# Performance work log

Hardware: AMD Instinct MI355X
Metric: run time of the kernel (lower is better)

Reference implementation:

```python
import jax, jax.numpy as jnp
import numpy as np

N_QUBITS = 8
N_LAYERS = 3
N_CLASSES = 3
BATCH = 16384


def setup_inputs() -> dict:
    key = jax.random.key(0)
    k1, k2, k3, k4 = jax.random.split(key, 4)
    x = jax.random.uniform(k1, (BATCH, N_QUBITS), dtype=jnp.float32)  # PCA feats in [0,1]
    q_weights = jax.random.normal(k2, (N_LAYERS * 2 * N_QUBITS,), dtype=jnp.float32) * 0.1
    W = jax.random.normal(k3, (N_CLASSES, N_CLASSES), dtype=jnp.float32) / np.sqrt(N_CLASSES)
    b = jax.random.normal(k4, (N_CLASSES,), dtype=jnp.float32) * 0.1
    return {"x": x, "q_weights": q_weights, "W": W, "b": b}


def _ry(state, wire, theta):
    """Batched RY(theta) on `wire`. state: (B,)+(2,)*n, theta: (B,)."""
    ax = 1 + wire
    s0 = jnp.take(state, 0, axis=ax)
    s1 = jnp.take(state, 1, axis=ax)
    bshape = (theta.shape[0],) + (1,) * (s0.ndim - 1)
    c = jnp.cos(0.5 * theta).reshape(bshape)
    s = jnp.sin(0.5 * theta).reshape(bshape)
    return jnp.stack([c * s0 - s * s1, s * s0 + c * s1], axis=ax)


def _rz(state, wire, theta):
    """RZ(theta) on `wire`, theta scalar: diag(e^{-i t/2}, e^{i t/2})."""
    ax = 1 + wire
    phases = jnp.stack([jnp.exp(-0.5j * theta), jnp.exp(0.5j * theta)])
    shape = (1,) * ax + (2,) + (1,) * (state.ndim - ax - 1)
    return state * phases.reshape(shape)


def _cnot(state, ctrl, tgt):
    """CNOT: flip target bit on the control=1 slice."""
    cax = 1 + ctrl
    a0 = jnp.take(state, 0, axis=cax)
    a1 = jnp.take(state, 1, axis=cax)
    # control axis was removed; target axis shifts down by one if tgt > ctrl
    tax = 1 + tgt if tgt < ctrl else tgt
    a1 = jnp.flip(a1, axis=tax)
    return jnp.stack([a0, a1], axis=cax)


def _circuit(x, q_weights):
    B = x.shape[0]
    state = jnp.zeros((B, 2 ** N_QUBITS), dtype=jnp.complex64).at[:, 0].set(1.0)
    state = state.reshape((B,) + (2,) * N_QUBITS)
    for layer in range(N_LAYERS):
        base = layer * 2 * N_QUBITS
        for i in range(N_QUBITS):
            state = _ry(state, i, x[:, i] * np.pi + q_weights[base + i])
        for i in range(N_QUBITS - 1):
            state = _cnot(state, i, i + 1)
        state = _cnot(state, N_QUBITS - 1, 0)
        for i in range(N_QUBITS):
            state = _rz(state, i, q_weights[base + N_QUBITS + i])
    probs = state.real ** 2 + state.imag ** 2  # (B,)+(2,)*n
    zs = []
    for i in range(N_CLASSES):
        ax = 1 + i
        p = probs.sum(axis=tuple(a for a in range(1, N_QUBITS + 1) if a != ax))  # (B,2)
        zs.append(p[:, 0] - p[:, 1])  # <Z_i>
    return jnp.stack(zs, axis=1).astype(jnp.float32)  # (B, n_classes)


def reference(x, q_weights, W, b):
    q_out = _circuit(x, q_weights)
    return q_out @ W.T + b
```

## Files before the change

### kernel.cpp

```cpp
#include <hip/hip_runtime.h>
#include <math.h>

#define NQ 8
#define NL 3
#define NC 3
#define BATCH 16384


__device__ __forceinline__ int par(int x) { return __popc(x) & 1; }

template<int CTRL>
__device__ __forceinline__ float dppmov(float v) {
  return __builtin_bit_cast(float,
    __builtin_amdgcn_update_dpp(0, __builtin_bit_cast(int, v), CTRL, 0xF, 0xF, true));
}

template<int M>
__device__ __forceinline__ float xl(float v) {
  if constexpr (M >= 16) {
    return __builtin_bit_cast(float,
      __builtin_amdgcn_ds_swizzle(__builtin_bit_cast(int, v), (M << 10) | 0x1F));
  } else {
    constexpr int hi = M & 12;
    constexpr int first = (hi == 0) ? 0 : (hi == 4) ? 0x141
                          : (hi == 8) ? 0x128
                          : 0x140;
    constexpr int qx = (hi == 4 || hi == 12) ? ((M & 3) ^ 3) : (M & 3);
    constexpr int qc = (qx == 1) ? 0xB1 : (qx == 2) ? 0x4E : 0x1B;
    float t = v;
    if constexpr (first != 0) t = dppmov<first>(t);
    if constexpr (qx != 0)    t = dppmov<qc>(t);
    return t;
  }
}

template<int UREG, int GREG, int GLANE>
__device__ __forceinline__ void ry_rr(float (&sr)[8], float (&si)[8],
                                      float c, float s, int q) {
  const float sl = par(q & GLANE) ? s : -s;
  #pragma unroll
  for (int rA = 0; rA < 8; ++rA) {
    if (rA < (rA ^ UREG)) {
      const int rB = rA ^ UREG;
      const float FA = par(rA & GREG) ? -sl : sl;
      const float ar = sr[rA], ai = si[rA];
      sr[rA] = c * ar + FA * sr[rB];
      si[rA] = c * ai + FA * si[rB];
      sr[rB] = c * sr[rB] - FA * ar;
      si[rB] = c * si[rB] - FA * ai;
    }
  }
}

template<int ULANE, int GREG, int GLANE>
__device__ __forceinline__ void ry_ll(float (&sr)[8], float (&si)[8],
                                      float c, float s, int q) {
  const float sl = par(q & GLANE) ? s : -s;
  #pragma unroll
  for (int r = 0; r < 8; ++r) {
    const float xr = xl<ULANE>(sr[r]);
    const float xi = xl<ULANE>(si[r]);
    const float F  = par(r & GREG) ? -sl : sl;
    sr[r] = c * sr[r] + F * xr;
    si[r] = c * si[r] + F * xi;
  }
}

template<int UREG, int ULANE, int GREG, int GLANE>
__device__ __forceinline__ void ry_mix(float (&sr)[8], float (&si)[8],
                                       float c, float s, int q) {
  constexpr int RFLIP = __builtin_popcount(GREG & UREG) & 1;
  const float sl = par(q & GLANE) ? s : -s;
  #pragma unroll
  for (int rA = 0; rA < 8; ++rA) {
    if (rA < (rA ^ UREG)) {
      const int rB = rA ^ UREG;
      const float pBr = xl<ULANE>(sr[rB]);
      const float pBi = xl<ULANE>(si[rB]);
      const float pAr = xl<ULANE>(sr[rA]);
      const float pAi = xl<ULANE>(si[rA]);
      const float FA = par(rA & GREG) ? -sl : sl;
      const float FB = RFLIP ? -FA : FA;
      sr[rA] = c * sr[rA] + FA * pBr;
      si[rA] = c * si[rA] + FA * pBi;
      sr[rB] = c * sr[rB] + FB * pAr;
      si[rB] = c * si[rB] + FB * pAi;
    }
  }
}

__global__ __launch_bounds__(256, 8) void vqc_kernel(
    const float* __restrict__ x, const float* __restrict__ qw,
    const float* __restrict__ W, const float* __restrict__ b,
    float* __restrict__ out)
{
  const int tid  = threadIdx.x;
  const int q    = tid & 31;
  const int elem = blockIdx.x * 8 + (tid >> 5);

  const float PI = 3.14159265358979323846f;

  float xs[8];
  {
    const float4 x0 = *(const float4*)(x + elem * 8);
    const float4 x1 = *(const float4*)(x + elem * 8 + 4);
    xs[0] = x0.x; xs[1] = x0.y; xs[2] = x0.z; xs[3] = x0.w;
    xs[4] = x1.x; xs[5] = x1.y; xs[6] = x1.z; xs[7] = x1.w;
  }

  float sr[8], si[8];

  {
    float cw[8], sv[8];
    #pragma unroll
    for (int w = 0; w < 8; ++w)
      __sincosf(0.5f * (PI * xs[w] + qw[w]), &sv[w], &cw[w]);

    float P = ((q & 1)  ? sv[3] : cw[3]);
    P      *= ((q & 2)  ? sv[4] : cw[4]);
    P      *= ((q & 4)  ? sv[5] : cw[5]);
    P      *= ((q & 8)  ? sv[6] : cw[6]);
    P      *= ((q & 16) ? sv[7] : cw[7]);
    sr[0] = P * cw[0];
    sr[1] = P * sv[0];
    #pragma unroll
    for (int r = 0; r < 2; ++r) { sr[r + 2] = sr[r] * sv[1]; sr[r] *= cw[1]; }
    #pragma unroll
    for (int r = 0; r < 4; ++r) { sr[r + 4] = sr[r] * sv[2]; sr[r] *= cw[2]; }
  }

  {
    const float h0 = 0.5f * qw[8],  h1 = 0.5f * qw[9];
    const float h2 = 0.5f * qw[10], h3 = 0.5f * qw[11];
    const float h4 = 0.5f * qw[12], h5 = 0.5f * qw[13];
    const float h6 = 0.5f * qw[14], h7 = 0.5f * qw[15];
    const float a0 = par(q & 31) ? h0 : -h0;
    const float a1 = -h1;
    const float A7 = -h2 + (par(q & 1)  ? h3 : -h3) + (par(q & 3)  ? h4 : -h4)
                         + (par(q & 7)  ? h5 : -h5) + (par(q & 15) ? h6 : -h6)
                         + (par(q & 31) ? h7 : -h7);
    float cp[8], sp[8];
    #pragma unroll
    for (int r = 0; r < 8; ++r) {
      if (!(r & 2)) {
        const float phi = (par(r & 6) ? -a0 : a0) + (par(r & 3) ? -a1 : a1)
                        + (par(r & 7) ? -A7 : A7);
        float s_, c_;
        __sincosf(phi, &s_, &c_);
        cp[r] = c_;     sp[r] = s_;
        cp[r ^ 2] = c_; sp[r ^ 2] = -s_;
      }
    }
    #pragma unroll
    for (int r = 0; r < 8; ++r) { si[r] = sp[r] * sr[r]; sr[r] = cp[r] * sr[r]; }
  }

  {
    float cw[8], sv[8];
    #pragma unroll
    for (int w = 0; w < 8; ++w)
      __sincosf(0.5f * (PI * xs[w] + qw[16 + w]), &sv[w], &cw[w]);

    ry_rr <3,     6, 31>(sr, si, cw[0], sv[0], q);
    ry_rr <6,     3,  0>(sr, si, cw[1], sv[1], q);
    ry_mix<4, 1,  7,  0>(sr, si, cw[2], sv[2], q);
    ry_ll <3,     7,  1>(sr, si, cw[3], sv[3], q);
    ry_ll <6,     7,  3>(sr, si, cw[4], sv[4], q);
    ry_ll <12,    7,  7>(sr, si, cw[5], sv[5], q);
    ry_ll <24,    7, 15>(sr, si, cw[6], sv[6], q);
    ry_mix<3, 16, 7, 31>(sr, si, cw[7], sv[7], q);
  }

  {
    const float h0 = 0.5f * qw[24], h1 = 0.5f * qw[25];
    const float h2 = 0.5f * qw[26], h3 = 0.5f * qw[27];
    const float h4 = 0.5f * qw[28], h5 = 0.5f * qw[29];
    const float h6 = 0.5f * qw[30], h7 = 0.5f * qw[31];
    const float a0 = par(q & 21) ? h0 : -h0;
    const float A5 = (par(q & 31) ? h1 : -h1) + (par(q & 30) ? h3 : -h3)
                   + (par(q & 26) ? h5 : -h5) + (par(q & 10) ? h7 : -h7);
    const float A2 = (par(q & 31) ? h2 : -h2) + (par(q & 29) ? h4 : -h4)
                   + (par(q & 21) ? h6 : -h6);
    float cp[8], sp[8];
    #pragma unroll
    for (int r = 0; r < 4; ++r) {
      const float phi = (par(r & 3) ? -a0 : a0) + (par(r & 5) ? -A5 : A5)
                      + (par(r & 2) ? -A2 : A2);
      float s_, c_;
      __sincosf(phi, &s_, &c_);
      cp[r] = c_;     sp[r] = s_;
      cp[r ^ 6] = c_; sp[r ^ 6] = -s_;
    }
    #pragma unroll
    for (int r = 0; r < 8; ++r) {
      const float re = sr[r], im = si[r];
      sr[r] = cp[r] * re - sp[r] * im;
      si[r] = cp[r] * im + sp[r] * re;
    }
  }

  {
    float cw[8], sv[8];
    #pragma unroll
    for (int w = 0; w < 8; ++w)
      __sincosf(0.5f * (PI * xs[w] + qw[32 + w]), &sv[w], &cw[w]);

    ry_rr <5,     3, 21>(sr, si, cw[0], sv[0], q);
    ry_mix<2, 1,  5, 31>(sr, si, cw[1], sv[1], q);
    ry_mix<4, 2,  2, 31>(sr, si, cw[2], sv[2], q);
    ry_ll <5,     5, 30>(sr, si, cw[3], sv[3], q);
    ry_ll <10,    2, 29>(sr, si, cw[4], sv[4], q);
    ry_ll <20,    5, 26>(sr, si, cw[5], sv[5], q);
    ry_mix<3, 8,  2, 21>(sr, si, cw[6], sv[6], q);
    ry_mix<6, 16, 5, 10>(sr, si, cw[7], sv[7], q);
  }

  float z0 = 0.f, z1 = 0.f, z2 = 0.f;
  #pragma unroll
  for (int r = 0; r < 8; ++r) {
    const float p = sr[r] * sr[r] + si[r] * si[r];
    z0 += par(r & 2) ? -p : p;
    z1 += par(r & 6) ? -p : p;
    z2 += par(r & 4) ? -p : p;
  }
  if (par(q & 6))  z0 = -z0;
  if (par(q & 10)) z1 = -z1;
  if (par(q & 21)) z2 = -z2;

  z0 += xl<1>(z0);  z1 += xl<1>(z1);  z2 += xl<1>(z2);
  z0 += xl<2>(z0);  z1 += xl<2>(z1);  z2 += xl<2>(z2);
  z0 += xl<4>(z0);  z1 += xl<4>(z1);  z2 += xl<4>(z2);
  z0 += xl<8>(z0);  z1 += xl<8>(z1);  z2 += xl<8>(z2);
  z0 += xl<16>(z0); z1 += xl<16>(z1); z2 += xl<16>(z2);

  if (q < NC) {
    out[elem * NC + q] = b[q] + W[q * 3 + 0] * z0 + W[q * 3 + 1] * z1
                              + W[q * 3 + 2] * z2;
  }
}

extern "C" void kernel_launch(void* const* d_in, const int* in_sizes, int n_in,
                              void* d_out, int out_size, void* d_ws, size_t ws_size,
                              hipStream_t stream) {
  const float* x  = (const float*)d_in[0];
  const float* qw = (const float*)d_in[1];
  const float* W  = (const float*)d_in[2];
  const float* b  = (const float*)d_in[3];
  float* out = (float*)d_out;

  dim3 grid(BATCH / 8);
  vqc_kernel<<<grid, 256, 0, stream>>>(x, qw, W, b, out);
}
```

Baseline: 22.94 us.

## Split state 16 registers x 16 lanes per batch element, drop ds_swizzle

Changes the per-element statevector layout from 8 registers across 32 lanes to 16 registers across 16 lanes, so every cross-lane exchange is done with DPP alone and the ds_swizzle path goes away. The gate wire mappings and phase and sign bookkeeping are redone for the new split, and each block now handles 16 batch elements. Launch bounds drop to 4 waves per SIMD to allow the larger register footprint. This trades fewer lane exchanges and more per-thread ILP for higher register pressure and lower occupancy.

```diff
diff --git a/kernel.cpp b/kernel.cpp
--- a/kernel.cpp
+++ b/kernel.cpp
@@ -17,32 +17,30 @@
 
 template<int M>
 __device__ __forceinline__ float xl(float v) {
-  if constexpr (M >= 16) {
-    return __builtin_bit_cast(float,
-      __builtin_amdgcn_ds_swizzle(__builtin_bit_cast(int, v), (M << 10) | 0x1F));
-  } else {
-    constexpr int hi = M & 12;
-    constexpr int first = (hi == 0) ? 0 : (hi == 4) ? 0x141
-                          : (hi == 8) ? 0x128
-                          : 0x140;
-    constexpr int qx = (hi == 4 || hi == 12) ? ((M & 3) ^ 3) : (M & 3);
-    constexpr int qc = (qx == 1) ? 0xB1 : (qx == 2) ? 0x4E : 0x1B;
-    float t = v;
-    if constexpr (first != 0) t = dppmov<first>(t);
-    if constexpr (qx != 0)    t = dppmov<qc>(t);
-    return t;
-  }
-}
+  static_assert(M > 0 && M < 16, "DPP-only exchange");
+  constexpr int hi = M & 12;
+  constexpr int first = (hi == 0) ? 0 : (hi == 4) ? 0x141
+                        : (hi == 8) ? 0x128
+                        : 0x140;
+  constexpr int qx = (hi == 4 || hi == 12) ? ((M & 3) ^ 3) : (M & 3);
+  constexpr int qc = (qx == 1) ? 0xB1 : (qx == 2) ? 0x4E : 0x1B;
+  float t = v;
+  if constexpr (first != 0) t = dppmov<first>(t);
+  if constexpr (qx != 0)    t = dppmov<qc>(t);
+  return t;
+}
+
 
 template<int UREG, int GREG, int GLANE>
-__device__ __forceinline__ void ry_rr(float (&sr)[8], float (&si)[8],
+__device__ __forceinline__ void ry_rr(float (&sr)[16], float (&si)[16],
                                       float c, float s, int q) {
+  static_assert((__builtin_popcount(UREG & GREG) & 1) == 1, "<g,u>!=1");
   const float sl = par(q & GLANE) ? s : -s;
   #pragma unroll
-  for (int rA = 0; rA < 8; ++rA) {
+  for (int rA = 0; rA < 16; ++rA) {
     if (rA < (rA ^ UREG)) {
       const int rB = rA ^ UREG;
-      const float FA = par(rA & GREG) ? -sl : sl;
+      const float FA = (__builtin_popcount(rA & GREG) & 1) ? -sl : sl;
       const float ar = sr[rA], ai = si[rA];
       sr[rA] = c * ar + FA * sr[rB];
       si[rA] = c * ai + FA * si[rB];
@@ -53,33 +51,36 @@
 }
 
 template<int ULANE, int GREG, int GLANE>
-__device__ __forceinline__ void ry_ll(float (&sr)[8], float (&si)[8],
+__device__ __forceinline__ void ry_ll(float (&sr)[16], float (&si)[16],
                                       float c, float s, int q) {
+  static_assert((__builtin_popcount(ULANE & GLANE) & 1) == 1, "<g,u>!=1");
   const float sl = par(q & GLANE) ? s : -s;
   #pragma unroll
-  for (int r = 0; r < 8; ++r) {
+  for (int r = 0; r < 16; ++r) {
     const float xr = xl<ULANE>(sr[r]);
     const float xi = xl<ULANE>(si[r]);
-    const float F  = par(r & GREG) ? -sl : sl;
+    const float F  = (__builtin_popcount(r & GREG) & 1) ? -sl : sl;
     sr[r] = c * sr[r] + F * xr;
     si[r] = c * si[r] + F * xi;
   }
 }
 
 template<int UREG, int ULANE, int GREG, int GLANE>
-__device__ __forceinline__ void ry_mix(float (&sr)[8], float (&si)[8],
+__device__ __forceinline__ void ry_mix(float (&sr)[16], float (&si)[16],
                                        float c, float s, int q) {
+  static_assert(((__builtin_popcount(UREG & GREG) + __builtin_popcount(ULANE & GLANE)) & 1) == 1,
+                "<g,u>!=1");
   constexpr int RFLIP = __builtin_popcount(GREG & UREG) & 1;
   const float sl = par(q & GLANE) ? s : -s;
   #pragma unroll
-  for (int rA = 0; rA < 8; ++rA) {
+  for (int rA = 0; rA < 16; ++rA) {
     if (rA < (rA ^ UREG)) {
       const int rB = rA ^ UREG;
       const float pBr = xl<ULANE>(sr[rB]);
       const float pBi = xl<ULANE>(si[rB]);
       const float pAr = xl<ULANE>(sr[rA]);
       const float pAi = xl<ULANE>(si[rA]);
-      const float FA = par(rA & GREG) ? -sl : sl;
+      const float FA = (__builtin_popcount(rA & GREG) & 1) ? -sl : sl;
       const float FB = RFLIP ? -FA : FA;
       sr[rA] = c * sr[rA] + FA * pBr;
       si[rA] = c * si[rA] + FA * pBi;
@@ -89,14 +90,14 @@
   }
 }
 
-__global__ __launch_bounds__(256, 8) void vqc_kernel(
+__global__ __launch_bounds__(256, 4) void vqc_kernel(
     const float* __restrict__ x, const float* __restrict__ qw,
     const float* __restrict__ W, const float* __restrict__ b,
     float* __restrict__ out)
 {
   const int tid  = threadIdx.x;
-  const int q    = tid & 31;
-  const int elem = blockIdx.x * 8 + (tid >> 5);
+  const int q    = tid & 15;
+  const int elem = blockIdx.x * 16 + (tid >> 4);
 
   const float PI = 3.14159265358979323846f;
 
@@ -108,25 +109,26 @@
     xs[4] = x1.x; xs[5] = x1.y; xs[6] = x1.z; xs[7] = x1.w;
   }
 
-  float sr[8], si[8];
-
-  {
-    float cw[8], sv[8];
+  float sr[16], si[16];
+
+  {
+    float cw[8], sw[8];
     #pragma unroll
     for (int w = 0; w < 8; ++w)
-      __sincosf(0.5f * (PI * xs[w] + qw[w]), &sv[w], &cw[w]);
-
-    float P = ((q & 1)  ? sv[3] : cw[3]);
-    P      *= ((q & 2)  ? sv[4] : cw[4]);
-    P      *= ((q & 4)  ? sv[5] : cw[5]);
-    P      *= ((q & 8)  ? sv[6] : cw[6]);
-    P      *= ((q & 16) ? sv[7] : cw[7]);
+      __sincosf(0.5f * (PI * xs[w] + qw[w]), &sw[w], &cw[w]);
+
+    float P = ((q & 1) ? sw[4] : cw[4]);
+    P      *= ((q & 2) ? sw[5] : cw[5]);
+    P      *= ((q & 4) ? sw[6] : cw[6]);
+    P      *= ((q & 8) ? sw[7] : cw[7]);
     sr[0] = P * cw[0];
-    sr[1] = P * sv[0];
-    #pragma unroll
-    for (int r = 0; r < 2; ++r) { sr[r + 2] = sr[r] * sv[1]; sr[r] *= cw[1]; }
-    #pragma unroll
-    for (int r = 0; r < 4; ++r) { sr[r + 4] = sr[r] * sv[2]; sr[r] *= cw[2]; }
+    sr[1] = P * sw[0];
+    #pragma unroll
+    for (int r = 0; r < 2; ++r) { sr[r + 2] = sr[r] * sw[1]; sr[r] *= cw[1]; }
+    #pragma unroll
+    for (int r = 0; r < 4; ++r) { sr[r + 4] = sr[r] * sw[2]; sr[r] *= cw[2]; }
+    #pragma unroll
+    for (int r = 0; r < 8; ++r) { sr[r + 8] = sr[r] * sw[3]; sr[r] *= cw[3]; }
   }
 
   {
@@ -134,17 +136,19 @@
     const float h2 = 0.5f * qw[10], h3 = 0.5f * qw[11];
     const float h4 = 0.5f * qw[12], h5 = 0.5f * qw[13];
     const float h6 = 0.5f * qw[14], h7 = 0.5f * qw[15];
-    const float a0 = par(q & 31) ? h0 : -h0;
-    const float a1 = -h1;
-    const float A7 = -h2 + (par(q & 1)  ? h3 : -h3) + (par(q & 3)  ? h4 : -h4)
-                         + (par(q & 7)  ? h5 : -h5) + (par(q & 15) ? h6 : -h6)
-                         + (par(q & 31) ? h7 : -h7);
-    float cp[8], sp[8];
-    #pragma unroll
-    for (int r = 0; r < 8; ++r) {
+    const float c0 = par(q & 15) ? h0 : -h0;
+    const float c1 = -h1;
+    const float c2 = -h2;
+    const float A  = -h3 + (par(q & 1) ? h4 : -h4) + (par(q & 3)  ? h5 : -h5)
+                         + (par(q & 7) ? h6 : -h6) + (par(q & 15) ? h7 : -h7);
+    float cp[16], sp[16];
+    #pragma unroll
+    for (int r = 0; r < 16; ++r) {
       if (!(r & 2)) {
-        const float phi = (par(r & 6) ? -a0 : a0) + (par(r & 3) ? -a1 : a1)
-                        + (par(r & 7) ? -A7 : A7);
+        const float phi = ((__builtin_popcount(r & 14) & 1) ? -c0 : c0)
+                        + ((__builtin_popcount(r & 3)  & 1) ? -c1 : c1)
+                        + ((__builtin_popcount(r & 7)  & 1) ? -c2 : c2)
+                        + ((__builtin_popcount(r & 15) & 1) ? -A  : A);
         float s_, c_;
         __sincosf(phi, &s_, &c_);
         cp[r] = c_;     sp[r] = s_;
@@ -152,23 +156,23 @@
       }
     }
     #pragma unroll
-    for (int r = 0; r < 8; ++r) { si[r] = sp[r] * sr[r]; sr[r] = cp[r] * sr[r]; }
-  }
-
-  {
-    float cw[8], sv[8];
+    for (int r = 0; r < 16; ++r) { si[r] = sp[r] * sr[r]; sr[r] = cp[r] * sr[r]; }
+  }
+
+  {
+    float cw[8], sw[8];
     #pragma unroll
     for (int w = 0; w < 8; ++w)
-      __sincosf(0.5f * (PI * xs[w] + qw[16 + w]), &sv[w], &cw[w]);
-
-    ry_rr <3,     6, 31>(sr, si, cw[0], sv[0], q);
-    ry_rr <6,     3,  0>(sr, si, cw[1], sv[1], q);
-    ry_mix<4, 1,  7,  0>(sr, si, cw[2], sv[2], q);
-    ry_ll <3,     7,  1>(sr, si, cw[3], sv[3], q);
-    ry_ll <6,     7,  3>(sr, si, cw[4], sv[4], q);
-    ry_ll <12,    7,  7>(sr, si, cw[5], sv[5], q);
-    ry_ll <24,    7, 15>(sr, si, cw[6], sv[6], q);
-    ry_mix<3, 16, 7, 31>(sr, si, cw[7], sv[7], q);
+      __sincosf(0.5f * (PI * xs[w] + qw[16 + w]), &sw[w], &cw[w]);
+
+    ry_rr <3,    14, 15>(sr, si, cw[0], sw[0], q);
+    ry_rr <6,     3,  0>(sr, si, cw[1], sw[1], q);
+    ry_rr <12,    7,  0>(sr, si, cw[2], sw[2], q);
+    ry_mix<8, 1, 15,  0>(sr, si, cw[3], sw[3], q);
+    ry_ll <3,    15,  1>(sr, si, cw[4], sw[4], q);
+    ry_ll <6,    15,  3>(sr, si, cw[5], sw[5], q);
+    ry_ll <12,   15,  7>(sr, si, cw[6], sw[6], q);
+    ry_mix<3, 8, 15, 15>(sr, si, cw[7], sw[7], q);
   }
 
   {
@@ -176,23 +180,28 @@
     const float h2 = 0.5f * qw[26], h3 = 0.5f * qw[27];
     const float h4 = 0.5f * qw[28], h5 = 0.5f * qw[29];
     const float h6 = 0.5f * qw[30], h7 = 0.5f * qw[31];
-    const float a0 = par(q & 21) ? h0 : -h0;
-    const float A5 = (par(q & 31) ? h1 : -h1) + (par(q & 30) ? h3 : -h3)
-                   + (par(q & 26) ? h5 : -h5) + (par(q & 10) ? h7 : -h7);
-    const float A2 = (par(q & 31) ? h2 : -h2) + (par(q & 29) ? h4 : -h4)
-                   + (par(q & 21) ? h6 : -h6);
-    float cp[8], sp[8];
-    #pragma unroll
-    for (int r = 0; r < 4; ++r) {
-      const float phi = (par(r & 3) ? -a0 : a0) + (par(r & 5) ? -A5 : A5)
-                      + (par(r & 2) ? -A2 : A2);
-      float s_, c_;
-      __sincosf(phi, &s_, &c_);
-      cp[r] = c_;     sp[r] = s_;
-      cp[r ^ 6] = c_; sp[r ^ 6] = -s_;
-    }
-    #pragma unroll
-    for (int r = 0; r < 8; ++r) {
+    const float d0 = par(q & 10) ? h0 : -h0;
+    const float d1 = par(q & 15) ? h1 : -h1;
+    const float d2 = (par(q & 15) ? h2 : -h2) + (par(q & 14) ? h4 : -h4)
+                   + (par(q & 10) ? h6 : -h6);
+    const float d3 = (par(q & 15) ? h3 : -h3) + (par(q & 13) ? h5 : -h5)
+                   + (par(q & 5)  ? h7 : -h7);
+    float cp[16], sp[16];
+    #pragma unroll
+    for (int r = 0; r < 16; ++r) {
+      if (!(r & 2)) {
+        const float phi = ((__builtin_popcount(r & 11) & 1) ? -d0 : d0)
+                        + ((__builtin_popcount(r & 13) & 1) ? -d1 : d1)
+                        + ((__builtin_popcount(r & 10) & 1) ? -d2 : d2)
+                        + ((__builtin_popcount(r & 5)  & 1) ? -d3 : d3);
+        float s_, c_;
+        __sincosf(phi, &s_, &c_);
+        cp[r] = c_;     sp[r] = s_;
+        cp[r ^ 6] = c_; sp[r ^ 6] = -s_;
+      }
+    }
+    #pragma unroll
+    for (int r = 0; r < 16; ++r) {
       const float re = sr[r], im = si[r];
       sr[r] = cp[r] * re - sp[r] * im;
       si[r] = cp[r] * im + sp[r] * re;
@@ -200,38 +209,37 @@
   }
 
   {
-    float cw[8], sv[8];
+    float cw[8], sw[8];
     #pragma unroll
     for (int w = 0; w < 8; ++w)
-      __sincosf(0.5f * (PI * xs[w] + qw[32 + w]), &sv[w], &cw[w]);
-
-    ry_rr <5,     3, 21>(sr, si, cw[0], sv[0], q);
-    ry_mix<2, 1,  5, 31>(sr, si, cw[1], sv[1], q);
-    ry_mix<4, 2,  2, 31>(sr, si, cw[2], sv[2], q);
-    ry_ll <5,     5, 30>(sr, si, cw[3], sv[3], q);
-    ry_ll <10,    2, 29>(sr, si, cw[4], sv[4], q);
-    ry_ll <20,    5, 26>(sr, si, cw[5], sv[5], q);
-    ry_mix<3, 8,  2, 21>(sr, si, cw[6], sv[6], q);
-    ry_mix<6, 16, 5, 10>(sr, si, cw[7], sv[7], q);
+      __sincosf(0.5f * (PI * xs[w] + qw[32 + w]), &sw[w], &cw[w]);
+
+    ry_rr <5,    11, 10>(sr, si, cw[0], sw[0], q);
+    ry_rr <10,   13, 15>(sr, si, cw[1], sw[1], q);
+    ry_mix<4, 1, 10, 15>(sr, si, cw[2], sw[2], q);
+    ry_mix<8, 2,  5, 15>(sr, si, cw[3], sw[3], q);
+    ry_ll <5,    10, 14>(sr, si, cw[4], sw[4], q);
+    ry_ll <10,    5, 13>(sr, si, cw[5], sw[5], q);
+    ry_mix<3, 4, 10, 10>(sr, si, cw[6], sw[6], q);
+    ry_mix<6, 8,  5,  5>(sr, si, cw[7], sw[7], q);
   }
 
   float z0 = 0.f, z1 = 0.f, z2 = 0.f;
   #pragma unroll
-  for (int r = 0; r < 8; ++r) {
+  for (int r = 0; r < 16; ++r) {
     const float p = sr[r] * sr[r] + si[r] * si[r];
-    z0 += par(r & 2) ? -p : p;
-    z1 += par(r & 6) ? -p : p;
-    z2 += par(r & 4) ? -p : p;
-  }
-  if (par(q & 6))  z0 = -z0;
-  if (par(q & 10)) z1 = -z1;
-  if (par(q & 21)) z2 = -z2;
-
-  z0 += xl<1>(z0);  z1 += xl<1>(z1);  z2 += xl<1>(z2);
-  z0 += xl<2>(z0);  z1 += xl<2>(z1);  z2 += xl<2>(z2);
-  z0 += xl<4>(z0);  z1 += xl<4>(z1);  z2 += xl<4>(z2);
-  z0 += xl<8>(z0);  z1 += xl<8>(z1);  z2 += xl<8>(z2);
-  z0 += xl<16>(z0); z1 += xl<16>(z1); z2 += xl<16>(z2);
+    z0 += (__popc(r & 2)  & 1) ? -p : p;
+    z1 += (__popc(r & 6)  & 1) ? -p : p;
+    z2 += (__popc(r & 12) & 1) ? -p : p;
+  }
+  if (par(q & 3))  z0 = -z0;
+  if (par(q & 5))  z1 = -z1;
+  if (par(q & 10)) z2 = -z2;
+
+  z0 += xl<1>(z0); z1 += xl<1>(z1); z2 += xl<1>(z2);
+  z0 += xl<2>(z0); z1 += xl<2>(z1); z2 += xl<2>(z2);
+  z0 += xl<4>(z0); z1 += xl<4>(z1); z2 += xl<4>(z2);
+  z0 += xl<8>(z0); z1 += xl<8>(z1); z2 += xl<8>(z2);
 
   if (q < NC) {
     out[elem * NC + q] = b[q] + W[q * 3 + 0] * z0 + W[q * 3 + 1] * z1
@@ -248,6 +256,6 @@
   const float* b  = (const float*)d_in[3];
   float* out = (float*)d_out;
 
-  dim3 grid(BATCH / 8);
+  dim3 grid(BATCH / 16);
   vqc_kernel<<<grid, 256, 0, stream>>>(x, qw, W, b, out);
 }
```

Result: faster. 22.05 us (-3.9%).

## Spread each batch element's state vector across a full 64-lane wavefront

Applied to the files above, without the earlier changes.

Each batch element's 256-amplitude state now lives across 64 lanes with 4 complex registers per lane, where before it used 32 lanes with 8 registers. All gate bit mappings, phase parities and the expectation reduction are rederived for the new layout, and a ds_bpermute path is added for cross-half lane exchanges. Blocks now hold 4 elements, so the grid doubles. The aim is fewer registers and less serial work per lane. In exchange, each element costs twice the lanes and there are more cross-lane shuffles, including a slower bpermute stage, plus lower launch_bounds occupancy.

```diff
diff --git a/kernel.cpp b/kernel.cpp
--- a/kernel.cpp
+++ b/kernel.cpp
@@ -17,10 +17,8 @@
 
 template<int M>
 __device__ __forceinline__ float xl(float v) {
-  if constexpr (M >= 16) {
-    return __builtin_bit_cast(float,
-      __builtin_amdgcn_ds_swizzle(__builtin_bit_cast(int, v), (M << 10) | 0x1F));
-  } else {
+  static_assert(M > 0 && M < 64, "mask range");
+  if constexpr (M < 16) {
     constexpr int hi = M & 12;
     constexpr int first = (hi == 0) ? 0 : (hi == 4) ? 0x141
                           : (hi == 8) ? 0x128
@@ -31,18 +29,27 @@
     if constexpr (first != 0) t = dppmov<first>(t);
     if constexpr (qx != 0)    t = dppmov<qc>(t);
     return t;
-  }
-}
+  } else if constexpr (M < 32) {
+    return __builtin_bit_cast(float,
+      __builtin_amdgcn_ds_swizzle(__builtin_bit_cast(int, v), (M << 10) | 0x1F));
+  } else {
+    const int li = (int)(threadIdx.x & 63);
+    return __builtin_bit_cast(float,
+      __builtin_amdgcn_ds_bpermute(((li ^ M) << 2), __builtin_bit_cast(int, v)));
+  }
+}
+
 
 template<int UREG, int GREG, int GLANE>
-__device__ __forceinline__ void ry_rr(float (&sr)[8], float (&si)[8],
+__device__ __forceinline__ void ry_rr(float (&sr)[4], float (&si)[4],
                                       float c, float s, int q) {
+  static_assert((__builtin_popcount(UREG & GREG) & 1) == 1, "<g,u>!=1");
   const float sl = par(q & GLANE) ? s : -s;
   #pragma unroll
-  for (int rA = 0; rA < 8; ++rA) {
+  for (int rA = 0; rA < 4; ++rA) {
     if (rA < (rA ^ UREG)) {
       const int rB = rA ^ UREG;
-      const float FA = par(rA & GREG) ? -sl : sl;
+      const float FA = (__builtin_popcount(rA & GREG) & 1) ? -sl : sl;
       const float ar = sr[rA], ai = si[rA];
       sr[rA] = c * ar + FA * sr[rB];
       si[rA] = c * ai + FA * si[rB];
@@ -53,33 +60,36 @@
 }
 
 template<int ULANE, int GREG, int GLANE>
-__device__ __forceinline__ void ry_ll(float (&sr)[8], float (&si)[8],
+__device__ __forceinline__ void ry_ll(float (&sr)[4], float (&si)[4],
                                       float c, float s, int q) {
+  static_assert((__builtin_popcount(ULANE & GLANE) & 1) == 1, "<g,u>!=1");
   const float sl = par(q & GLANE) ? s : -s;
   #pragma unroll
-  for (int r = 0; r < 8; ++r) {
+  for (int r = 0; r < 4; ++r) {
     const float xr = xl<ULANE>(sr[r]);
     const float xi = xl<ULANE>(si[r]);
-    const float F  = par(r & GREG) ? -sl : sl;
+    const float F  = (__builtin_popcount(r & GREG) & 1) ? -sl : sl;
     sr[r] = c * sr[r] + F * xr;
     si[r] = c * si[r] + F * xi;
   }
 }
 
 template<int UREG, int ULANE, int GREG, int GLANE>
-__device__ __forceinline__ void ry_mix(float (&sr)[8], float (&si)[8],
+__device__ __forceinline__ void ry_mix(float (&sr)[4], float (&si)[4],
                                        float c, float s, int q) {
+  static_assert(((__builtin_popcount(UREG & GREG) + __builtin_popcount(ULANE & GLANE)) & 1) == 1,
+                "<g,u>!=1");
   constexpr int RFLIP = __builtin_popcount(GREG & UREG) & 1;
   const float sl = par(q & GLANE) ? s : -s;
   #pragma unroll
-  for (int rA = 0; rA < 8; ++rA) {
+  for (int rA = 0; rA < 4; ++rA) {
     if (rA < (rA ^ UREG)) {
       const int rB = rA ^ UREG;
       const float pBr = xl<ULANE>(sr[rB]);
       const float pBi = xl<ULANE>(si[rB]);
       const float pAr = xl<ULANE>(sr[rA]);
       const float pAi = xl<ULANE>(si[rA]);
-      const float FA = par(rA & GREG) ? -sl : sl;
+      const float FA = (__builtin_popcount(rA & GREG) & 1) ? -sl : sl;
       const float FB = RFLIP ? -FA : FA;
       sr[rA] = c * sr[rA] + FA * pBr;
       si[rA] = c * si[rA] + FA * pBi;
@@ -89,14 +99,14 @@
   }
 }
 
-__global__ __launch_bounds__(256, 8) void vqc_kernel(
+__global__ __launch_bounds__(256, 6) void vqc_kernel(
     const float* __restrict__ x, const float* __restrict__ qw,
     const float* __restrict__ W, const float* __restrict__ b,
     float* __restrict__ out)
 {
   const int tid  = threadIdx.x;
-  const int q    = tid & 31;
-  const int elem = blockIdx.x * 8 + (tid >> 5);
+  const int q    = tid & 63;
+  const int elem = blockIdx.x * 4 + (tid >> 6);
 
   const float PI = 3.14159265358979323846f;
 
@@ -108,25 +118,23 @@
     xs[4] = x1.x; xs[5] = x1.y; xs[6] = x1.z; xs[7] = x1.w;
   }
 
-  float sr[8], si[8];
-
-  {
-    float cw[8], sv[8];
+  float sr[4], si[4];
+
+  {
+    float c0_, s0_, c1_, s1_;
+    __sincosf(0.5f * (PI * xs[0] + qw[0]), &s0_, &c0_);
+    __sincosf(0.5f * (PI * xs[1] + qw[1]), &s1_, &c1_);
+    float P = 1.f;
     #pragma unroll
-    for (int w = 0; w < 8; ++w)
-      __sincosf(0.5f * (PI * xs[w] + qw[w]), &sv[w], &cw[w]);
-
-    float P = ((q & 1)  ? sv[3] : cw[3]);
-    P      *= ((q & 2)  ? sv[4] : cw[4]);
-    P      *= ((q & 4)  ? sv[5] : cw[5]);
-    P      *= ((q & 8)  ? sv[6] : cw[6]);
-    P      *= ((q & 16) ? sv[7] : cw[7]);
-    sr[0] = P * cw[0];
-    sr[1] = P * sv[0];
-    #pragma unroll
-    for (int r = 0; r < 2; ++r) { sr[r + 2] = sr[r] * sv[1]; sr[r] *= cw[1]; }
-    #pragma unroll
-    for (int r = 0; r < 4; ++r) { sr[r + 4] = sr[r] * sv[2]; sr[r] *= cw[2]; }
+    for (int w = 2; w < 8; ++w) {
+      float s_, c_;
+      __sincosf(0.5f * (PI * xs[w] + qw[w]), &s_, &c_);
+      P *= ((q >> (w - 2)) & 1) ? s_ : c_;
+    }
+    sr[0] = P * c0_ * c1_;
+    sr[1] = P * s0_ * c1_;
+    sr[2] = P * c0_ * s1_;
+    sr[3] = P * s0_ * s1_;
   }
 
   {
@@ -134,41 +142,29 @@
     const float h2 = 0.5f * qw[10], h3 = 0.5f * qw[11];
     const float h4 = 0.5f * qw[12], h5 = 0.5f * qw[13];
     const float h6 = 0.5f * qw[14], h7 = 0.5f * qw[15];
-    const float a0 = par(q & 31) ? h0 : -h0;
-    const float a1 = -h1;
-    const float A7 = -h2 + (par(q & 1)  ? h3 : -h3) + (par(q & 3)  ? h4 : -h4)
-                         + (par(q & 7)  ? h5 : -h5) + (par(q & 15) ? h6 : -h6)
-                         + (par(q & 31) ? h7 : -h7);
-    float cp[8], sp[8];
-    #pragma unroll
-    for (int r = 0; r < 8; ++r) {
-      if (!(r & 2)) {
-        const float phi = (par(r & 6) ? -a0 : a0) + (par(r & 3) ? -a1 : a1)
-                        + (par(r & 7) ? -A7 : A7);
-        float s_, c_;
-        __sincosf(phi, &s_, &c_);
-        cp[r] = c_;     sp[r] = s_;
-        cp[r ^ 2] = c_; sp[r ^ 2] = -s_;
-      }
-    }
-    #pragma unroll
-    for (int r = 0; r < 8; ++r) { si[r] = sp[r] * sr[r]; sr[r] = cp[r] * sr[r]; }
-  }
-
-  {
-    float cw[8], sv[8];
-    #pragma unroll
-    for (int w = 0; w < 8; ++w)
-      __sincosf(0.5f * (PI * xs[w] + qw[16 + w]), &sv[w], &cw[w]);
-
-    ry_rr <3,     6, 31>(sr, si, cw[0], sv[0], q);
-    ry_rr <6,     3,  0>(sr, si, cw[1], sv[1], q);
-    ry_mix<4, 1,  7,  0>(sr, si, cw[2], sv[2], q);
-    ry_ll <3,     7,  1>(sr, si, cw[3], sv[3], q);
-    ry_ll <6,     7,  3>(sr, si, cw[4], sv[4], q);
-    ry_ll <12,    7,  7>(sr, si, cw[5], sv[5], q);
-    ry_ll <24,    7, 15>(sr, si, cw[6], sv[6], q);
-    ry_mix<3, 16, 7, 31>(sr, si, cw[7], sv[7], q);
+    const float a0 = par(q & 63) ? h0 : -h0;
+    const float B  = -h1 + (par(q & 1)  ? h2 : -h2) + (par(q & 3)  ? h3 : -h3)
+                         + (par(q & 7)  ? h4 : -h4) + (par(q & 15) ? h5 : -h5)
+                         + (par(q & 31) ? h6 : -h6) + (par(q & 63) ? h7 : -h7);
+    float sp0, cp0, sp1, cp1;
+    __sincosf(a0 + B, &sp0, &cp0);
+    __sincosf(a0 - B, &sp1, &cp1);
+    si[0] =  sp0 * sr[0]; sr[0] *= cp0;
+    si[1] =  sp1 * sr[1]; sr[1] *= cp1;
+    si[2] = -sp0 * sr[2]; sr[2] *= cp0;
+    si[3] = -sp1 * sr[3]; sr[3] *= cp1;
+  }
+
+  {
+    float c_, s_;
+    __sincosf(0.5f * (PI * xs[0] + qw[16]), &s_, &c_); ry_rr <3,     2, 63>(sr, si, c_, s_, q);
+    __sincosf(0.5f * (PI * xs[1] + qw[17]), &s_, &c_); ry_mix<2, 1,  3,  0>(sr, si, c_, s_, q);
+    __sincosf(0.5f * (PI * xs[2] + qw[18]), &s_, &c_); ry_ll <3,     3,  1>(sr, si, c_, s_, q);
+    __sincosf(0.5f * (PI * xs[3] + qw[19]), &s_, &c_); ry_ll <6,     3,  3>(sr, si, c_, s_, q);
+    __sincosf(0.5f * (PI * xs[4] + qw[20]), &s_, &c_); ry_ll <12,    3,  7>(sr, si, c_, s_, q);
+    __sincosf(0.5f * (PI * xs[5] + qw[21]), &s_, &c_); ry_ll <24,    3, 15>(sr, si, c_, s_, q);
+    __sincosf(0.5f * (PI * xs[6] + qw[22]), &s_, &c_); ry_ll <48,    3, 31>(sr, si, c_, s_, q);
+    __sincosf(0.5f * (PI * xs[7] + qw[23]), &s_, &c_); ry_mix<3, 32, 3, 63>(sr, si, c_, s_, q);
   }
 
   {
@@ -176,62 +172,51 @@
     const float h2 = 0.5f * qw[26], h3 = 0.5f * qw[27];
     const float h4 = 0.5f * qw[28], h5 = 0.5f * qw[29];
     const float h6 = 0.5f * qw[30], h7 = 0.5f * qw[31];
-    const float a0 = par(q & 21) ? h0 : -h0;
-    const float A5 = (par(q & 31) ? h1 : -h1) + (par(q & 30) ? h3 : -h3)
-                   + (par(q & 26) ? h5 : -h5) + (par(q & 10) ? h7 : -h7);
-    const float A2 = (par(q & 31) ? h2 : -h2) + (par(q & 29) ? h4 : -h4)
-                   + (par(q & 21) ? h6 : -h6);
-    float cp[8], sp[8];
+    const float t0 = par(q & 42) ? h0 : -h0;
+    const float D1 = (par(q & 63) ? h1 : -h1) + (par(q & 61) ? h3 : -h3)
+                   + (par(q & 53) ? h5 : -h5) + (par(q & 21) ? h7 : -h7);
+    const float D2 = (par(q & 62) ? h2 : -h2) + (par(q & 58) ? h4 : -h4)
+                   + (par(q & 42) ? h6 : -h6);
+    const float ph[4] = { t0 + D1 + D2, -t0 - D1 + D2,
+                          -t0 + D1 - D2,  t0 - D1 - D2 };
     #pragma unroll
     for (int r = 0; r < 4; ++r) {
-      const float phi = (par(r & 3) ? -a0 : a0) + (par(r & 5) ? -A5 : A5)
-                      + (par(r & 2) ? -A2 : A2);
-      float s_, c_;
-      __sincosf(phi, &s_, &c_);
-      cp[r] = c_;     sp[r] = s_;
-      cp[r ^ 6] = c_; sp[r ^ 6] = -s_;
-    }
-    #pragma unroll
-    for (int r = 0; r < 8; ++r) {
+      float sp, cp;
+      __sincosf(ph[r], &sp, &cp);
       const float re = sr[r], im = si[r];
-      sr[r] = cp[r] * re - sp[r] * im;
-      si[r] = cp[r] * im + sp[r] * re;
-    }
-  }
-
-  {
-    float cw[8], sv[8];
-    #pragma unroll
-    for (int w = 0; w < 8; ++w)
-      __sincosf(0.5f * (PI * xs[w] + qw[32 + w]), &sv[w], &cw[w]);
-
-    ry_rr <5,     3, 21>(sr, si, cw[0], sv[0], q);
-    ry_mix<2, 1,  5, 31>(sr, si, cw[1], sv[1], q);
-    ry_mix<4, 2,  2, 31>(sr, si, cw[2], sv[2], q);
-    ry_ll <5,     5, 30>(sr, si, cw[3], sv[3], q);
-    ry_ll <10,    2, 29>(sr, si, cw[4], sv[4], q);
-    ry_ll <20,    5, 26>(sr, si, cw[5], sv[5], q);
-    ry_mix<3, 8,  2, 21>(sr, si, cw[6], sv[6], q);
-    ry_mix<6, 16, 5, 10>(sr, si, cw[7], sv[7], q);
-  }
-
-  float z0 = 0.f, z1 = 0.f, z2 = 0.f;
-  #pragma unroll
-  for (int r = 0; r < 8; ++r) {
-    const float p = sr[r] * sr[r] + si[r] * si[r];
-    z0 += par(r & 2) ? -p : p;
-    z1 += par(r & 6) ? -p : p;
-    z2 += par(r & 4) ? -p : p;
-  }
-  if (par(q & 6))  z0 = -z0;
-  if (par(q & 10)) z1 = -z1;
-  if (par(q & 21)) z2 = -z2;
+      sr[r] = cp * re - sp * im;
+      si[r] = cp * im + sp * re;
+    }
+  }
+
+  {
+    float c_, s_;
+    __sincosf(0.5f * (PI * xs[0] + qw[32]), &s_, &c_); ry_mix<1, 1,  3, 42>(sr, si, c_, s_, q);
+    __sincosf(0.5f * (PI * xs[1] + qw[33]), &s_, &c_); ry_mix<2, 2,  1, 63>(sr, si, c_, s_, q);
+    __sincosf(0.5f * (PI * xs[2] + qw[34]), &s_, &c_); ry_ll <5,     2, 62>(sr, si, c_, s_, q);
+    __sincosf(0.5f * (PI * xs[3] + qw[35]), &s_, &c_); ry_ll <10,    1, 61>(sr, si, c_, s_, q);
+    __sincosf(0.5f * (PI * xs[4] + qw[36]), &s_, &c_); ry_ll <20,    2, 58>(sr, si, c_, s_, q);
+    __sincosf(0.5f * (PI * xs[5] + qw[37]), &s_, &c_); ry_ll <40,    1, 53>(sr, si, c_, s_, q);
+    __sincosf(0.5f * (PI * xs[6] + qw[38]), &s_, &c_); ry_mix<3, 16, 2, 42>(sr, si, c_, s_, q);
+    __sincosf(0.5f * (PI * xs[7] + qw[39]), &s_, &c_); ry_mix<2, 33, 1, 21>(sr, si, c_, s_, q);
+  }
+
+  const float p0 = sr[0] * sr[0] + si[0] * si[0];
+  const float p1 = sr[1] * sr[1] + si[1] * si[1];
+  const float p2 = sr[2] * sr[2] + si[2] * si[2];
+  const float p3 = sr[3] * sr[3] + si[3] * si[3];
+  const float ta = (p0 + p1) - (p2 + p3);
+  const float tb =  p0 + p1 + p2 + p3;
+  float z0 = par(q & 12) ? -ta : ta;
+  float z1 = par(q & 21) ? -ta : ta;
+  float z2 = par(q & 43) ? -tb : tb;
 
   z0 += xl<1>(z0);  z1 += xl<1>(z1);  z2 += xl<1>(z2);
   z0 += xl<2>(z0);  z1 += xl<2>(z1);  z2 += xl<2>(z2);
   z0 += xl<4>(z0);  z1 += xl<4>(z1);  z2 += xl<4>(z2);
   z0 += xl<8>(z0);  z1 += xl<8>(z1);  z2 += xl<8>(z2);
   z0 += xl<16>(z0); z1 += xl<16>(z1); z2 += xl<16>(z2);
+  z0 += xl<32>(z0); z1 += xl<32>(z1); z2 += xl<32>(z2);
 
   if (q < NC) {
     out[elem * NC + q] = b[q] + W[q * 3 + 0] * z0 + W[q * 3 + 1] * z1
@@ -248,6 +233,6 @@
   const float* b  = (const float*)d_in[3];
   float* out = (float*)d_out;
 
-  dim3 grid(BATCH / 8);
+  dim3 grid(BATCH / 4);
   vqc_kernel<<<grid, 256, 0, stream>>>(x, qw, W, b, out);
 }
```

Measured after the change: 26.48 us. 15.4% more time.
